# Optimization experiments

Measured on AMD Instinct MI355X. Metric: run time of the kernel, lower is better.

Reference implementation:

```python
import jax, jax.numpy as jnp
import numpy as np

H, DK, DV, SEG, D = 16, 64, 64, 512, 1024


def setup_inputs() -> dict:
    key = jax.random.key(0)
    ks = jax.random.split(key, 6)
    B, T = 2, 8192
    x = jax.random.normal(ks[0], (B, T, D), jnp.float32)
    Wq = jax.random.normal(ks[1], (H * DK, D), jnp.float32) * 0.02
    Wk = jax.random.normal(ks[2], (H * DK, D), jnp.float32) * 0.02
    Wv = jax.random.normal(ks[3], (H * DV, D), jnp.float32) * 0.02
    Wout = jax.random.normal(ks[4], (D, H * DV), jnp.float32) * 0.02
    betas = jax.random.normal(ks[5], (1, H, 1, DV), jnp.float32)
    return {"x": x, "Wq": Wq, "Wk": Wk, "Wv": Wv, "Wout": Wout, "betas": betas}


def reference(x, Wq, Wk, Wv, Wout, betas):
    B, T, _ = x.shape
    n_seg = T // SEG
    # Projections for the whole sequence, then PyTorch-style .view head split:
    # per segment, (B, SEG, H*dk).view(B, H, SEG, dk) is a raw row-major reshape.
    q = (x @ Wq.T).reshape(B, n_seg, H, SEG, DK)
    k = (x @ Wk.T).reshape(B, n_seg, H, SEG, DK)
    v = (x @ Wv.T).reshape(B, n_seg, H, SEG, DV)
    qs = jnp.moveaxis(q, 1, 0)  # (n_seg, B, H, SEG, DK)
    ks_ = jnp.moveaxis(k, 1, 0)
    vs = jnp.moveaxis(v, 1, 0)

    gate = jax.nn.sigmoid(betas)                 # (1, H, 1, DV)
    scale = 1.0 / jnp.sqrt(jnp.float32(DK))

    mem0 = jnp.zeros((B, H, DK, DV), x.dtype)
    # z broadcasts from (B,H,DV,1) to (B,H,DV,DK) on first update; start dense.
    z0 = jnp.zeros((B, H, DV, DK), x.dtype)

    def step(carry, seg):
        mem, z = carry
        q, k, v = seg
        sq = jax.nn.elu(q) + 1.0                 # (B,H,S,DK)
        sk = jax.nn.elu(k) + 1.0
        z = z + sk.sum(axis=-2, keepdims=True)   # (B,H,DV,DK) via broadcast
        scores = jnp.einsum('bhsd,bhtd->bhst', q, k) * scale
        att_dot = jnp.einsum('bhst,bhtv->bhsv', jax.nn.softmax(scores, axis=-1), v)
        att_mem = jnp.einsum('bhsd,bhdv->bhsv', sq, mem) / jnp.einsum('bhsd,bhdv->bhsv', sq, z)
        mem = mem + jnp.einsum('bhsd,bhsv->bhdv', sk, v)  # linear update (after att_mem)
        att = gate * att_mem + (1.0 - gate) * att_dot     # (B,H,S,DV)
        # PyTorch .view(B, SEG, H*DV) on (B,H,S,DV): raw reshape, no transpose.
        y = att.reshape(B, SEG, H * DV) @ Wout.T          # (B,SEG,D)
        return (mem, z), y

    (_, _), ys = jax.lax.scan(step, (mem0, z0), (qs, ks_, vs))
    out = jnp.moveaxis(ys, 0, 1).reshape(B, T, D)
    return out
```

## Files before the change

### kernel.cpp

```cpp
#include <hip/hip_runtime.h>


#define H_ 16
#define SEG_ 512
#define NSEG_ 16
#define B_ 2
#define T_ 8192
#define D_ 1024
#define BT_ 16384

#define NPROJ ((size_t)BT_ * D_)
#define NW ((size_t)D_ * D_)

__device__ unsigned short g_qb[NPROJ], g_kb[NPROJ], g_vb[NPROJ];
__device__ unsigned short g_xh[NPROJ];
__device__ unsigned short g_wqkv[3 * NW];
__device__ unsigned short g_ath[NPROJ], g_atl[NPROJ];
__device__ unsigned short g_woh[NW], g_wol[NW];
__device__ unsigned short g_vt[(size_t)512 * 64 * 512];
__device__ float g_M[(size_t)512 * 4096];
__device__ float g_z[(size_t)512 * 64];

typedef __attribute__((ext_vector_type(8))) short short8;
typedef __attribute__((ext_vector_type(8))) unsigned short ushort8;
typedef __attribute__((ext_vector_type(4))) float f32x4;

__device__ __forceinline__ float elu1(float x) {
    return x > 0.f ? x + 1.f : __expf(x);
}
__device__ __forceinline__ unsigned short f2bf(float x) {
    unsigned u = __float_as_uint(x);
    u += 0x7fffu + ((u >> 16) & 1u);
    return (unsigned short)(u >> 16);
}
__device__ __forceinline__ float bf2f(unsigned short h) {
    return __uint_as_float((unsigned)h << 16);
}
__device__ __forceinline__ void load_lds16(const unsigned short* g, unsigned short* l) {
    __builtin_amdgcn_global_load_lds(
        (const __attribute__((address_space(1))) unsigned int*)g,
        (__attribute__((address_space(3))) unsigned int*)l, 16, 0, 0);
}
__device__ __forceinline__ int sz8(int row, int blk) {
    return row * 64 + ((blk ^ (row & 7)) << 3);
}

__global__ __launch_bounds__(256) void prep_cast(
    const float* __restrict__ x, const float* __restrict__ Wq,
    const float* __restrict__ Wk, const float* __restrict__ Wv,
    const float* __restrict__ Wout,
    unsigned short* __restrict__ xh, unsigned short* __restrict__ wqkv,
    unsigned short* __restrict__ woh, unsigned short* __restrict__ wol)
{
    const int b = blockIdx.x;
    const int nXB = (int)(NPROJ / 1024);
    const int nWB = (int)(NW / 1024);
    if (b < nXB + 3 * nWB) {
        const float* in;
        unsigned short* out;
        int i;
        if (b < nXB) {
            in = x; out = xh; i = (b * 256 + threadIdx.x) * 4;
        } else {
            const int wsel = (b - nXB) / nWB;
            const int wb   = (b - nXB) % nWB;
            in  = wsel == 0 ? Wq : (wsel == 1 ? Wk : Wv);
            out = wqkv + (size_t)wsel * NW;
            i = (wb * 256 + threadIdx.x) * 4;
        }
        float4 v = *(const float4*)(in + i);
        ushort4 h;
        h.x = f2bf(v.x); h.y = f2bf(v.y); h.z = f2bf(v.z); h.w = f2bf(v.w);
        *(ushort4*)(out + i) = h;
    } else {
        const int wb = b - nXB - 3 * nWB;
        const int i = (wb * 256 + threadIdx.x) * 4;
        float4 v = *(const float4*)(Wout + i);
        ushort4 h, l;
        h.x = f2bf(v.x); l.x = f2bf(v.x - bf2f(h.x));
        h.y = f2bf(v.y); l.y = f2bf(v.y - bf2f(h.y));
        h.z = f2bf(v.z); l.z = f2bf(v.z - bf2f(h.z));
        h.w = f2bf(v.w); l.w = f2bf(v.w - bf2f(h.w));
        *(ushort4*)(woh + i) = h;
        *(ushort4*)(wol + i) = l;
    }
}


#define VMC(N) asm volatile("s_waitcnt vmcnt(" #N ")" ::: "memory")

#define STAGE_A(p, h, tt, u) \
    load_lds16(Aw + ((h) * 128 + (u) * 8) * 1024 + (tt) * 64, \
               &lds[(p) * 32768 + ((h) * 128 + w * 16 + (u) * 8) * 64])
#define STAGE_B(p, h, tt, u) \
    load_lds16(Bww + ((h) * 128 + (u) * 8) * 1024 + (tt) * 64, \
               &lds[(p) * 32768 + 16384 + ((h) * 128 + w * 16 + (u) * 8) * 64])
#define STAGE_AH(p, h, tt) do { STAGE_A(p, h, tt, 0); STAGE_A(p, h, tt, 1); } while (0)
#define STAGE_BH(p, h, tt) do { STAGE_B(p, h, tt, 0); STAGE_B(p, h, tt, 1); } while (0)

#define LDA(PBUF, MLO) do { \
    _Pragma("unroll") for (int m2 = 0; m2 < 4; ++m2) \
    _Pragma("unroll") for (int ks2 = 0; ks2 < 2; ++ks2) \
        a[m2][ks2] = *(const short8*)&lds[(PBUF) * 32768 + aoff[ks2] + ((MLO) + m2) * 1024]; \
} while (0)

#define LDB(PBUF) do { \
    _Pragma("unroll") for (int n2 = 0; n2 < 4; ++n2) \
    _Pragma("unroll") for (int ks2 = 0; ks2 < 2; ++ks2) \
        b[n2][ks2] = *(const short8*)&lds[(PBUF) * 32768 + boff[ks2] + n2 * 1024]; \
} while (0)

#define MFMA_QUAD(MLO, NLO) do { \
    _Pragma("unroll") for (int m2 = 0; m2 < 4; ++m2) \
    _Pragma("unroll") for (int n2 = 0; n2 < 2; ++n2) \
    _Pragma("unroll") for (int ks2 = 0; ks2 < 2; ++ks2) \
        acc[(MLO) + m2][(NLO) + n2] = __builtin_amdgcn_mfma_f32_16x16x32_bf16( \
            a[m2][ks2], b[(NLO) + n2][ks2], acc[(MLO) + m2][(NLO) + n2], 0, 0, 0); \
} while (0)

#define PH(MLO, NLO) do { \
    __builtin_amdgcn_s_barrier(); \
    asm volatile("s_waitcnt lgkmcnt(0)" ::: "memory"); \
    __builtin_amdgcn_sched_barrier(0); \
    __builtin_amdgcn_s_setprio(1); \
    MFMA_QUAD(MLO, NLO); \
    __builtin_amdgcn_s_setprio(0); \
    __builtin_amdgcn_sched_barrier(0); \
    __builtin_amdgcn_s_barrier(); \
} while (0)

__global__ __launch_bounds__(512, 2) void gemm_qkv8(
    const unsigned short* __restrict__ A, const unsigned short* __restrict__ Bw,
    unsigned short* __restrict__ Q, unsigned short* __restrict__ Kp,
    unsigned short* __restrict__ V)
{
    __shared__ unsigned short lds[65536];
    const int t = threadIdx.x, lane = t & 63, w = t >> 6;
    const int wave_m = w >> 2, wave_n = w & 3;

    const int bid = blockIdx.x;
    const int sb = (bid & 7) * 96 + (bid >> 3);
    const int mb = sb / 12, nb = sb % 12;
    const int m0 = mb * 256, n0 = nb * 256;

    const int lrow = lane >> 3;
    const int lcol = ((lane & 7) ^ lrow) * 8;
    const unsigned short* Aw  = A  + (size_t)(m0 + w * 16 + lrow) * 1024 + lcol;
    const unsigned short* Bww = Bw + (size_t)(n0 + w * 16 + lrow) * 1024 + lcol;

    const int fr = lane & 15, g4 = lane >> 4;
    int aoff[2], boff[2];
#pragma unroll
    for (int ks2 = 0; ks2 < 2; ++ks2) {
        aoff[ks2] = (wave_m * 128 + fr) * 64 + (((ks2 * 4 + g4) ^ (fr & 7)) * 8);
        boff[ks2] = 16384 + (wave_n * 64 + fr) * 64 + (((ks2 * 4 + g4) ^ (fr & 7)) * 8);
    }

    f32x4 acc[8][4];
#pragma unroll
    for (int i = 0; i < 8; ++i)
#pragma unroll
        for (int j = 0; j < 4; ++j) acc[i][j] = (f32x4)0.f;
    short8 a[4][2], b[4][2];

    STAGE_BH(0, 0, 0); STAGE_BH(0, 1, 0); STAGE_AH(0, 0, 0); STAGE_AH(0, 1, 0);
    STAGE_BH(1, 0, 1); STAGE_BH(1, 1, 1); STAGE_AH(1, 0, 1);
    VMC(6);
    __builtin_amdgcn_s_barrier();

#pragma unroll 1
    for (int it = 0; it < 7; ++it) {
        const int t1 = 2 * it + 1, t2 = 2 * it + 2, t3 = 2 * it + 3;
        LDB(0); LDA(0, 0);
        STAGE_AH(1, 1, t1);
        PH(0, 0);
        STAGE_BH(0, 0, t2);
        PH(0, 2);
        LDA(0, 4);
        STAGE_BH(0, 1, t2);
        PH(4, 0);
        STAGE_AH(0, 0, t2);
        VMC(6);
        PH(4, 2);
        LDB(1); LDA(1, 0);
        STAGE_AH(0, 1, t2);
        PH(0, 0);
        STAGE_BH(1, 0, t3);
        PH(0, 2);
        LDA(1, 4);
        STAGE_BH(1, 1, t3);
        PH(4, 0);
        STAGE_AH(1, 0, t3);
        VMC(6);
        PH(4, 2);
    }
    LDB(0); LDA(0, 0);
    STAGE_AH(1, 1, 15);
    PH(0, 0);
    PH(0, 2);
    LDA(0, 4);
    PH(4, 0);
    VMC(0);
    PH(4, 2);
    LDB(1); LDA(1, 0);
    PH(0, 0);
    PH(0, 2);
    LDA(1, 4);
    PH(4, 0);
    PH(4, 2);

    const int ccol = lane & 15, crow = (lane >> 4) * 4;
#pragma unroll
    for (int m = 0; m < 8; ++m)
#pragma unroll
        for (int n = 0; n < 4; ++n) {
            const int col = wave_n * 64 + n * 16 + ccol;
            const int cb = col >> 3, cl = col & 7;
#pragma unroll
            for (int r = 0; r < 4; ++r) {
                const int row = wave_m * 128 + m * 16 + crow + r;
                lds[row * 256 + ((cb ^ (row & 31)) << 3) + cl] = f2bf(acc[m][n][r]);
            }
        }
    __syncthreads();
    const int which = n0 >> 10, col0 = n0 & 1023;
    unsigned short* outp = which == 0 ? Q : (which == 1 ? Kp : V);
    const int orow = t >> 1, och = (t & 1) * 128;
    unsigned short* gp = outp + (size_t)(m0 + orow) * 1024 + col0 + och;
#pragma unroll
    for (int u = 0; u < 128; u += 8) {
        const int bo = (och + u) >> 3;
        *(ushort8*)(gp + u) = *(const ushort8*)&lds[orow * 256 + ((bo ^ (orow & 31)) << 3)];
    }
}


#define OSTG(p, arrp, aroff, tt, u) \
    load_lds16(arrp + (size_t)(u) * 16 * 1024 + (tt) * 32, \
               &lds[(p) * 32768 + (aroff) + (w * 32 + (u) * 16) * 32])
#define OUNIT(p, arrp, aroff, tt) do { OSTG(p, arrp, aroff, tt, 0); OSTG(p, arrp, aroff, tt, 1); } while (0)

#define OLDA(PBUF, MLO) do { \
    _Pragma("unroll") for (int m2 = 0; m2 < 4; ++m2) { \
        ah[m2] = *(const short8*)&lds[(PBUF) * 32768 +         ao + ((MLO) + m2) * 512]; \
        al[m2] = *(const short8*)&lds[(PBUF) * 32768 +  8192 + ao + ((MLO) + m2) * 512]; \
    } \
} while (0)

#define OLDB(PBUF) do { \
    _Pragma("unroll") for (int n2 = 0; n2 < 4; ++n2) { \
        bh[n2] = *(const short8*)&lds[(PBUF) * 32768 + 16384 + bo + n2 * 512]; \
        bl[n2] = *(const short8*)&lds[(PBUF) * 32768 + 24576 + bo + n2 * 512]; \
    } \
} while (0)

#define OQUAD(MLO, NLO) do { \
    _Pragma("unroll") for (int m2 = 0; m2 < 4; ++m2) \
    _Pragma("unroll") for (int n2 = 0; n2 < 2; ++n2) { \
        acc[(MLO) + m2][(NLO) + n2] = __builtin_amdgcn_mfma_f32_16x16x32_bf16( \
            ah[m2], bh[(NLO) + n2], acc[(MLO) + m2][(NLO) + n2], 0, 0, 0); \
        acc[(MLO) + m2][(NLO) + n2] = __builtin_amdgcn_mfma_f32_16x16x32_bf16( \
            al[m2], bh[(NLO) + n2], acc[(MLO) + m2][(NLO) + n2], 0, 0, 0); \
        acc[(MLO) + m2][(NLO) + n2] = __builtin_amdgcn_mfma_f32_16x16x32_bf16( \
            ah[m2], bl[(NLO) + n2], acc[(MLO) + m2][(NLO) + n2], 0, 0, 0); \
    } \
} while (0)

#define OPH(MLO, NLO) do { \
    __builtin_amdgcn_s_barrier(); \
    asm volatile("s_waitcnt lgkmcnt(0)" ::: "memory"); \
    __builtin_amdgcn_sched_barrier(0); \
    __builtin_amdgcn_s_setprio(1); \
    OQUAD(MLO, NLO); \
    __builtin_amdgcn_s_setprio(0); \
    __builtin_amdgcn_sched_barrier(0); \
    __builtin_amdgcn_s_barrier(); \
} while (0)

__global__ __launch_bounds__(512, 2) void gemm_bt8(
    const unsigned short* __restrict__ Ah, const unsigned short* __restrict__ Al,
    const unsigned short* __restrict__ Bh, const unsigned short* __restrict__ Bl,
    float* __restrict__ C)
{
    __shared__ unsigned short lds[65536];
    const int t = threadIdx.x, lane = t & 63, w = t >> 6;
    const int wave_m = w >> 2, wave_n = w & 3;

    const int bid = blockIdx.x;
    const int sb = (bid & 7) * 32 + (bid >> 3);
    const int m0 = (sb >> 2) * 256, n0 = (sb & 3) * 256;

    const int lrow = lane >> 2;
    const int lcol = ((lane & 3) ^ ((lane >> 3) & 3)) * 8;
    const unsigned short* Ahp = Ah + (size_t)(m0 + w * 32 + lrow) * 1024 + lcol;
    const unsigned short* Alp = Al + (size_t)(m0 + w * 32 + lrow) * 1024 + lcol;
    const unsigned short* Bhp = Bh + (size_t)(n0 + w * 32 + lrow) * 1024 + lcol;
    const unsigned short* Blp = Bl + (size_t)(n0 + w * 32 + lrow) * 1024 + lcol;

    const int fr = lane & 15, g4 = lane >> 4;
    const int xo = (g4 ^ ((fr >> 1) & 3)) * 8;
    const int ao = (wave_m * 128 + fr) * 32 + xo;
    const int bo = (wave_n * 64 + fr) * 32 + xo;

    f32x4 acc[8][4];
#pragma unroll
    for (int i = 0; i < 8; ++i)
#pragma unroll
        for (int j = 0; j < 4; ++j) acc[i][j] = (f32x4)0.f;
    short8 ah[4], al[4], bh[4], bl[4];

    OUNIT(0, Bhp, 16384, 0); OUNIT(0, Blp, 24576, 0); OUNIT(0, Ahp, 0, 0); OUNIT(0, Alp, 8192, 0);
    OUNIT(1, Bhp, 16384, 1); OUNIT(1, Blp, 24576, 1); OUNIT(1, Ahp, 0, 1);
    VMC(6);
    __builtin_amdgcn_s_barrier();

#pragma unroll 1
    for (int it = 0; it < 15; ++it) {
        const int t1 = 2 * it + 1, t2 = 2 * it + 2, t3 = 2 * it + 3;
        OLDB(0); OLDA(0, 0);
        OUNIT(1, Alp, 8192, t1);
        OPH(0, 0);
        OUNIT(0, Bhp, 16384, t2);
        OPH(0, 2);
        OLDA(0, 4);
        OUNIT(0, Blp, 24576, t2);
        OPH(4, 0);
        OUNIT(0, Ahp, 0, t2);
        VMC(6);
        OPH(4, 2);
        OLDB(1); OLDA(1, 0);
        OUNIT(0, Alp, 8192, t2);
        OPH(0, 0);
        OUNIT(1, Bhp, 16384, t3);
        OPH(0, 2);
        OLDA(1, 4);
        OUNIT(1, Blp, 24576, t3);
        OPH(4, 0);
        OUNIT(1, Ahp, 0, t3);
        VMC(6);
        OPH(4, 2);
    }
    OLDB(0); OLDA(0, 0);
    OUNIT(1, Alp, 8192, 31);
    OPH(0, 0);
    OPH(0, 2);
    OLDA(0, 4);
    OPH(4, 0);
    VMC(0);
    OPH(4, 2);
    OLDB(1); OLDA(1, 0);
    OPH(0, 0);
    OPH(0, 2);
    OLDA(1, 4);
    OPH(4, 0);
    OPH(4, 2);

    const int ccol = lane & 15, crow = (lane >> 4) * 4;
#pragma unroll
    for (int m = 0; m < 8; ++m)
#pragma unroll
        for (int n = 0; n < 4; ++n) {
            float* cp = C + (size_t)(m0 + wave_m * 128 + m * 16 + crow) * 1024
                          + (n0 + wave_n * 64 + n * 16 + ccol);
#pragma unroll
            for (int r = 0; r < 4; ++r) cp[(size_t)r * 1024] = acc[m][n][r];
        }
}

__global__ __launch_bounds__(256) void seg_stats(
    const unsigned short* __restrict__ kproj, const unsigned short* __restrict__ vproj,
    float* __restrict__ Mseg, float* __restrict__ zsum,
    unsigned short* __restrict__ vtg)
{
    __shared__ float ks[64][68];
    __shared__ float vs[64][68];
    const int idx = blockIdx.x;
    const int seg = idx & 15;
    const int bh  = idx >> 4;
    const int h   = bh & 15;
    const int b   = bh >> 4;
    const size_t base = ((size_t)b * T_ + (size_t)seg * SEG_ + (size_t)h * 32) * D_;
    const unsigned short* kt = kproj + base;
    const unsigned short* vt = vproj + base;
    const int t  = threadIdx.x;
    const int d0 = (t >> 4) * 4;
    const int v0 = (t & 15) * 4;
    const int lr = t >> 2;
    const int lc = (t & 3) * 16;
    float acc[4][4];
#pragma unroll
    for (int i = 0; i < 4; ++i)
#pragma unroll
        for (int j = 0; j < 4; ++j) acc[i][j] = 0.f;
    float zacc = 0.f;

    for (int c0 = 0; c0 < SEG_; c0 += 64) {
        __syncthreads();
        {
            const unsigned short* kp = kt + (size_t)(c0 + lr) * 64 + lc;
            const unsigned short* vp = vt + (size_t)(c0 + lr) * 64 + lc;
            ushort8 k0 = *(const ushort8*)kp,       k1 = *(const ushort8*)(kp + 8);
            ushort8 v0v = *(const ushort8*)vp,      v1 = *(const ushort8*)(vp + 8);
#pragma unroll
            for (int e = 0; e < 8; ++e) {
                ks[lr][lc + e]     = elu1(bf2f(k0[e]));
                ks[lr][lc + 8 + e] = elu1(bf2f(k1[e]));
                vs[lr][lc + e]     = bf2f(v0v[e]);
                vs[lr][lc + 8 + e] = bf2f(v1[e]);
            }
        }
        __syncthreads();
#pragma unroll 8
        for (int i = 0; i < 64; ++i) {
            float a0 = ks[i][d0 + 0], a1 = ks[i][d0 + 1];
            float a2 = ks[i][d0 + 2], a3 = ks[i][d0 + 3];
            float b0 = vs[i][v0 + 0], b1 = vs[i][v0 + 1];
            float b2 = vs[i][v0 + 2], b3 = vs[i][v0 + 3];
            acc[0][0] += a0 * b0; acc[0][1] += a0 * b1; acc[0][2] += a0 * b2; acc[0][3] += a0 * b3;
            acc[1][0] += a1 * b0; acc[1][1] += a1 * b1; acc[1][2] += a1 * b2; acc[1][3] += a1 * b3;
            acc[2][0] += a2 * b0; acc[2][1] += a2 * b1; acc[2][2] += a2 * b2; acc[2][3] += a2 * b3;
            acc[3][0] += a3 * b0; acc[3][1] += a3 * b1; acc[3][2] += a3 * b2; acc[3][3] += a3 * b3;
        }
        if (t < 64) {
#pragma unroll 8
            for (int i = 0; i < 64; ++i) zacc += ks[i][t];
        }
        {
            ushort8 w0, w1;
#pragma unroll
            for (int i = 0; i < 8; ++i) w0[i] = f2bf(vs[lc + i][lr]);
#pragma unroll
            for (int i = 0; i < 8; ++i) w1[i] = f2bf(vs[lc + 8 + i][lr]);
            unsigned short* vo = vtg + ((size_t)idx * 64 + lr) * 512 + c0 + lc;
            *(ushort8*)vo       = w0;
            *(ushort8*)(vo + 8) = w1;
        }
    }
    float* Mout = Mseg + (size_t)idx * 4096;
#pragma unroll
    for (int i = 0; i < 4; ++i)
        *(float4*)(Mout + (size_t)(d0 + i) * 64 + v0) =
            make_float4(acc[i][0], acc[i][1], acc[i][2], acc[i][3]);
    if (t < 64) zsum[(size_t)idx * 64 + t] = zacc;
}

__global__ __launch_bounds__(256) void prefix_scan(
    float* __restrict__ M, float* __restrict__ z)
{
    const int blk = blockIdx.x;
    const int bh  = blk >> 2, sl = blk & 3;
    const int t   = threadIdx.x;
    const size_t off = (size_t)bh * NSEG_ * 4096 + (size_t)sl * 1024 + (size_t)t * 4;
    float4 run = make_float4(0.f, 0.f, 0.f, 0.f);
    float runz = 0.f;
    for (int seg = 0; seg < NSEG_; ++seg) {
        const size_t o = off + (size_t)seg * 4096;
        float4 m = *(const float4*)(M + o);
        *(float4*)(M + o) = run;
        run.x += m.x; run.y += m.y; run.z += m.z; run.w += m.w;
        if (sl == 0 && t < 64) {
            const size_t oz = ((size_t)bh * NSEG_ + seg) * 64 + t;
            runz += z[oz];
            z[oz] = runz;
        }
    }
}

__global__ __launch_bounds__(256) void attn_mfma(
    const unsigned short* __restrict__ qproj, const unsigned short* __restrict__ kproj,
    const unsigned short* __restrict__ vtg, const float* __restrict__ memb,
    const float* __restrict__ Zaf, const float* __restrict__ betas,
    unsigned short* __restrict__ ath, unsigned short* __restrict__ atl)
{
    __shared__ unsigned short sm_k[64 * 64];
    __shared__ unsigned short sm_v[64 * 64];
    __shared__ unsigned short sm_p[64 * 64];
    __shared__ float Zsh[64], gsh[64];

    const int idx  = blockIdx.x;
    const int qc   = (idx >> 3) & 7;
    const int rest = (idx >> 6) * 8 + (idx & 7);
    const int bh   = rest >> 4;
    const int seg  = rest & 15;
    const int h    = bh & 15;
    const int b    = bh >> 4;
    const size_t base = ((size_t)b * T_ + (size_t)seg * SEG_ + (size_t)h * 32) * D_;

    const int t    = threadIdx.x;
    const int lane = t & 63;
    const int w    = t >> 6;
    const int c16  = lane & 15;
    const int g4   = lane >> 4;
    const int lr   = t >> 2;
    const int lc   = (t & 3) * 16;

    const unsigned short* qt = qproj + base + (size_t)qc * 4096;
    const unsigned short* kt = kproj + base;
    const unsigned short* vt = vtg + (size_t)rest * (64 * 512);
    const float* mb = memb + (size_t)rest * 4096;

    if (t < 64) {
        Zsh[t] = Zaf[(size_t)rest * 64 + t];
        gsh[t] = 1.f / (1.f + __expf(-betas[h * 64 + t]));
    }

    short8 qh[2], sqh[2];
    float rowsum = 0.f;
#pragma unroll
    for (int ks = 0; ks < 2; ++ks) {
        const unsigned short* qp = qt + (size_t)(w * 16 + c16) * 64 + g4 * 8 + ks * 32;
        ushort8 qv = *(const ushort8*)qp;
        short8 qf, sf;
#pragma unroll
        for (int j = 0; j < 8; ++j) {
            float e = elu1(bf2f(qv[j]));
            rowsum += e;
            qf[j] = (short)qv[j];
            sf[j] = (short)f2bf(e);
        }
        qh[ks] = qf; sqh[ks] = sf;
    }
    rowsum += __shfl_xor(rowsum, 16);
    rowsum += __shfl_xor(rowsum, 32);

    {
        const float* mp = mb + (size_t)lr * 64 + lc;
#pragma unroll
        for (int u = 0; u < 4; ++u) {
            float4 m4 = *(const float4*)(mp + u * 4);
            sm_p[sz8(lc + u * 4 + 0, lr >> 3) + (lr & 7)] = f2bf(m4.x);
            sm_p[sz8(lc + u * 4 + 1, lr >> 3) + (lr & 7)] = f2bf(m4.y);
            sm_p[sz8(lc + u * 4 + 2, lr >> 3) + (lr & 7)] = f2bf(m4.z);
            sm_p[sz8(lc + u * 4 + 3, lr >> 3) + (lr & 7)] = f2bf(m4.w);
        }
    }
    __syncthreads();

    f32x4 numf[4];
#pragma unroll
    for (int nf = 0; nf < 4; ++nf) numf[nf] = (f32x4)0.f;
#pragma unroll
    for (int ks = 0; ks < 2; ++ks)
#pragma unroll
        for (int nf = 0; nf < 4; ++nf) {
            short8 bm = *(const short8*)&sm_p[sz8(nf * 16 + c16, g4 + ks * 4)];
            numf[nf] = __builtin_amdgcn_mfma_f32_16x16x32_bf16(sqh[ks], bm, numf[nf], 0, 0, 0);
        }

    short8 bones;
#pragma unroll
    for (int j = 0; j < 8; ++j) bones[j] = (short)0x3F80;

    f32x4 o[4];
#pragma unroll
    for (int nf = 0; nf < 4; ++nf) o[nf] = (f32x4)0.f;
    float mrow[4] = {-1e30f, -1e30f, -1e30f, -1e30f};
    float lrow[4] = {0.f, 0.f, 0.f, 0.f};

    for (int kb = 0; kb < 8; ++kb) {
        __syncthreads();
        {
            const unsigned short* kp = kt + (size_t)(kb * 64 + lr) * 64 + lc;
            *(ushort8*)&sm_k[sz8(lr, lc >> 3)]       = *(const ushort8*)kp;
            *(ushort8*)&sm_k[sz8(lr, (lc >> 3) + 1)] = *(const ushort8*)(kp + 8);
            const unsigned short* vp = vt + (size_t)lr * 512 + kb * 64 + lc;
            *(ushort8*)&sm_v[sz8(lr, lc >> 3)]       = *(const ushort8*)vp;
            *(ushort8*)&sm_v[sz8(lr, (lc >> 3) + 1)] = *(const ushort8*)(vp + 8);
        }
        __syncthreads();

        f32x4 s[4];
#pragma unroll
        for (int nf = 0; nf < 4; ++nf) s[nf] = (f32x4)0.f;
#pragma unroll
        for (int ks = 0; ks < 2; ++ks)
#pragma unroll
            for (int nf = 0; nf < 4; ++nf) {
                short8 bk = *(const short8*)&sm_k[sz8(nf * 16 + c16, g4 + ks * 4)];
                s[nf] = __builtin_amdgcn_mfma_f32_16x16x32_bf16(qh[ks], bk, s[nf], 0, 0, 0);
            }
#pragma unroll
        for (int nf = 0; nf < 4; ++nf) s[nf] *= 0.125f;

        float pmax[4];
#pragma unroll
        for (int r = 0; r < 4; ++r)
            pmax[r] = fmaxf(fmaxf(s[0][r], s[1][r]), fmaxf(s[2][r], s[3][r]));
        const bool ok = pmax[0] <= mrow[0] + 8.f && pmax[1] <= mrow[1] + 8.f &&
                        pmax[2] <= mrow[2] + 8.f && pmax[3] <= mrow[3] + 8.f;
        if (!__all(ok)) {
#pragma unroll
            for (int r = 0; r < 4; ++r) {
                float mx = pmax[r];
                mx = fmaxf(mx, __shfl_xor(mx, 1));
                mx = fmaxf(mx, __shfl_xor(mx, 2));
                mx = fmaxf(mx, __shfl_xor(mx, 4));
                mx = fmaxf(mx, __shfl_xor(mx, 8));
                const float mnew = fmaxf(mrow[r], mx);
                const float corr = __expf(mrow[r] - mnew);
                mrow[r] = mnew;
                lrow[r] *= corr;
#pragma unroll
                for (int nf = 0; nf < 4; ++nf) o[nf][r] *= corr;
            }
        }
#pragma unroll
        for (int nf = 0; nf < 4; ++nf)
#pragma unroll
            for (int r = 0; r < 4; ++r) {
                s[nf][r] = __expf(s[nf][r] - mrow[r]);
                sm_p[sz8(w * 16 + g4 * 4 + r, nf * 2 + (c16 >> 3)) + (c16 & 7)] =
                    f2bf(s[nf][r]);
            }

        f32x4 psum = (f32x4)0.f;
#pragma unroll
        for (int ks = 0; ks < 2; ++ks) {
            short8 pa = *(const short8*)&sm_p[sz8(w * 16 + c16, g4 + ks * 4)];
            psum = __builtin_amdgcn_mfma_f32_16x16x32_bf16(pa, bones, psum, 0, 0, 0);
#pragma unroll
            for (int nf = 0; nf < 4; ++nf) {
                short8 bv = *(const short8*)&sm_v[sz8(nf * 16 + c16, g4 + ks * 4)];
                o[nf] = __builtin_amdgcn_mfma_f32_16x16x32_bf16(pa, bv, o[nf], 0, 0, 0);
            }
        }
#pragma unroll
        for (int r = 0; r < 4; ++r) lrow[r] += psum[r];
    }

    __syncthreads();

    float rs[4], invl[4];
#pragma unroll
    for (int r = 0; r < 4; ++r) {
        rs[r]   = __shfl(rowsum, (g4 << 2) + r);
        invl[r] = 1.f / lrow[r];
    }
#pragma unroll
    for (int nf = 0; nf < 4; ++nf) {
        const int col = nf * 16 + c16;
        const float Zc = Zsh[col], gc = gsh[col];
        const float izc = 1.f / Zc;
#pragma unroll
        for (int r = 0; r < 4; ++r) {
            const float adot = o[nf][r] * invl[r];
            const float amem = numf[nf][r] * izc / rs[r];
            const float res  = gc * amem + (1.f - gc) * adot;
            const unsigned short hv = f2bf(res);
            const unsigned short lv = f2bf(res - bf2f(hv));
            const int row = w * 16 + g4 * 4 + r;
            const int so  = sz8(row, nf * 2 + (c16 >> 3)) + (c16 & 7);
            sm_k[so] = hv;
            sm_v[so] = lv;
        }
    }
    __syncthreads();
    {
        const size_t ob = base + (size_t)(qc * 64 + lr) * 64 + lc;
        *(ushort8*)(ath + ob)     = *(const ushort8*)&sm_k[sz8(lr, lc >> 3)];
        *(ushort8*)(ath + ob + 8) = *(const ushort8*)&sm_k[sz8(lr, (lc >> 3) + 1)];
        *(ushort8*)(atl + ob)     = *(const ushort8*)&sm_v[sz8(lr, lc >> 3)];
        *(ushort8*)(atl + ob + 8) = *(const ushort8*)&sm_v[sz8(lr, (lc >> 3) + 1)];
    }
}

extern "C" void kernel_launch(void* const* d_in, const int* in_sizes, int n_in,
                              void* d_out, int out_size, void* d_ws, size_t ws_size,
                              hipStream_t stream) {
    const float* x     = (const float*)d_in[0];
    const float* Wq    = (const float*)d_in[1];
    const float* Wk    = (const float*)d_in[2];
    const float* Wv    = (const float*)d_in[3];
    const float* Wout  = (const float*)d_in[4];
    const float* betas = (const float*)d_in[5];
    float* out = (float*)d_out;
    (void)d_ws; (void)ws_size;

    float *M, *z;
    unsigned short *qb, *kb, *vb, *xh, *wqkv, *vt, *ath, *atl, *woh, *wol;
    hipGetSymbolAddress((void**)&qb,   HIP_SYMBOL(g_qb));
    hipGetSymbolAddress((void**)&kb,   HIP_SYMBOL(g_kb));
    hipGetSymbolAddress((void**)&vb,   HIP_SYMBOL(g_vb));
    hipGetSymbolAddress((void**)&xh,   HIP_SYMBOL(g_xh));
    hipGetSymbolAddress((void**)&wqkv, HIP_SYMBOL(g_wqkv));
    hipGetSymbolAddress((void**)&vt,   HIP_SYMBOL(g_vt));
    hipGetSymbolAddress((void**)&ath,  HIP_SYMBOL(g_ath));
    hipGetSymbolAddress((void**)&atl,  HIP_SYMBOL(g_atl));
    hipGetSymbolAddress((void**)&woh,  HIP_SYMBOL(g_woh));
    hipGetSymbolAddress((void**)&wol,  HIP_SYMBOL(g_wol));
    hipGetSymbolAddress((void**)&M,    HIP_SYMBOL(g_M));
    hipGetSymbolAddress((void**)&z,    HIP_SYMBOL(g_z));

    const int nXB = (int)(NPROJ / 1024), nWB = (int)(NW / 1024);
    prep_cast<<<nXB + 4 * nWB, 256, 0, stream>>>(x, Wq, Wk, Wv, Wout,
                                                 xh, wqkv, woh, wol);

    gemm_qkv8<<<dim3(768), 512, 0, stream>>>(xh, wqkv, qb, kb, vb);
    seg_stats<<<B_ * H_ * NSEG_, 256, 0, stream>>>(kb, vb, M, z, vt);
    prefix_scan<<<B_ * H_ * 4, 256, 0, stream>>>(M, z);
    attn_mfma<<<B_ * H_ * NSEG_ * 8, 256, 0, stream>>>(qb, kb, vt, M, z, betas, ath, atl);
    gemm_bt8<<<dim3(256), 512, 0, stream>>>(ath, atl, woh, wol, out);
}
```

Measured before the change: 502.4 us.

## Compute segment K^T V statistics with bf16 MFMA using hi/lo split

The seg_stats kernel now computes the per-segment K^T V outer-product sum and the key column sums with bf16 MFMA instructions instead of scalar FP32 FMAs out of shared memory. elu(k)+1 is split into high and low bf16 parts to keep near-FP32 accuracy, the column sum is done as an MFMA against a vector of ones, and V is staged transposed in a swizzled bf16 layout that is reused for the V-transpose write. This cuts scalar ALU work and shared-memory traffic in a small kernel, at the cost of extra MFMAs for the lo term and a slight accuracy change.

Result: faster. 485.8 us (-3.3%).

```diff
diff --git a/kernel.cpp b/kernel.cpp
--- a/kernel.cpp
+++ b/kernel.cpp
@@ -372,8 +372,9 @@
     float* __restrict__ Mseg, float* __restrict__ zsum,
     unsigned short* __restrict__ vtg)
 {
-    __shared__ float ks[64][68];
-    __shared__ float vs[64][68];
+    __shared__ unsigned short sm_kh[64 * 64];
+    __shared__ unsigned short sm_kl[64 * 64];
+    __shared__ unsigned short sm_vt[64 * 64];
     const int idx = blockIdx.x;
     const int seg = idx & 15;
     const int bh  = idx >> 4;
@@ -382,66 +383,75 @@
     const size_t base = ((size_t)b * T_ + (size_t)seg * SEG_ + (size_t)h * 32) * D_;
     const unsigned short* kt = kproj + base;
     const unsigned short* vt = vproj + base;
-    const int t  = threadIdx.x;
-    const int d0 = (t >> 4) * 4;
-    const int v0 = (t & 15) * 4;
-    const int lr = t >> 2;
-    const int lc = (t & 3) * 16;
-    float acc[4][4];
-#pragma unroll
-    for (int i = 0; i < 4; ++i)
-#pragma unroll
-        for (int j = 0; j < 4; ++j) acc[i][j] = 0.f;
-    float zacc = 0.f;
+    const int t    = threadIdx.x;
+    const int lane = t & 63;
+    const int w    = t >> 6;
+    const int c16  = lane & 15;
+    const int g4   = lane >> 4;
+    const int lr   = t >> 2;
+    const int lc   = (t & 3) * 16;
+
+    short8 bones;
+#pragma unroll
+    for (int j = 0; j < 8; ++j) bones[j] = (short)0x3F80;
+
+    f32x4 acc[4];
+#pragma unroll
+    for (int nt = 0; nt < 4; ++nt) acc[nt] = (f32x4)0.f;
+    f32x4 zacc = (f32x4)0.f;
 
     for (int c0 = 0; c0 < SEG_; c0 += 64) {
         __syncthreads();
         {
-            const unsigned short* kp = kt + (size_t)(c0 + lr) * 64 + lc;
-            const unsigned short* vp = vt + (size_t)(c0 + lr) * 64 + lc;
-            ushort8 k0 = *(const ushort8*)kp,       k1 = *(const ushort8*)(kp + 8);
-            ushort8 v0v = *(const ushort8*)vp,      v1 = *(const ushort8*)(vp + 8);
+            const int row = c0 + lane;
+            const unsigned short* kp = kt + (size_t)row * 64 + w * 16;
+            const unsigned short* vp = vt + (size_t)row * 64 + w * 16;
+            ushort8 k0 = *(const ushort8*)kp, k1 = *(const ushort8*)(kp + 8);
+            ushort8 v0 = *(const ushort8*)vp, v1 = *(const ushort8*)(vp + 8);
+            const int tb = lane >> 3, tl = lane & 7;
 #pragma unroll
             for (int e = 0; e < 8; ++e) {
-                ks[lr][lc + e]     = elu1(bf2f(k0[e]));
-                ks[lr][lc + 8 + e] = elu1(bf2f(k1[e]));
-                vs[lr][lc + e]     = bf2f(v0v[e]);
-                vs[lr][lc + 8 + e] = bf2f(v1[e]);
+                const float f0 = elu1(bf2f(k0[e]));
+                const unsigned short h0 = f2bf(f0), l0 = f2bf(f0 - bf2f(h0));
+                const float f1 = elu1(bf2f(k1[e]));
+                const unsigned short h1 = f2bf(f1), l1 = f2bf(f1 - bf2f(h1));
+                const int a0 = sz8(w * 16 + e,     tb) + tl;
+                const int a1 = sz8(w * 16 + 8 + e, tb) + tl;
+                sm_kh[a0] = h0; sm_kl[a0] = l0; sm_vt[a0] = v0[e];
+                sm_kh[a1] = h1; sm_kl[a1] = l1; sm_vt[a1] = v1[e];
             }
         }
         __syncthreads();
-#pragma unroll 8
-        for (int i = 0; i < 64; ++i) {
-            float a0 = ks[i][d0 + 0], a1 = ks[i][d0 + 1];
-            float a2 = ks[i][d0 + 2], a3 = ks[i][d0 + 3];
-            float b0 = vs[i][v0 + 0], b1 = vs[i][v0 + 1];
-            float b2 = vs[i][v0 + 2], b3 = vs[i][v0 + 3];
-            acc[0][0] += a0 * b0; acc[0][1] += a0 * b1; acc[0][2] += a0 * b2; acc[0][3] += a0 * b3;
-            acc[1][0] += a1 * b0; acc[1][1] += a1 * b1; acc[1][2] += a1 * b2; acc[1][3] += a1 * b3;
-            acc[2][0] += a2 * b0; acc[2][1] += a2 * b1; acc[2][2] += a2 * b2; acc[2][3] += a2 * b3;
-            acc[3][0] += a3 * b0; acc[3][1] += a3 * b1; acc[3][2] += a3 * b2; acc[3][3] += a3 * b3;
-        }
-        if (t < 64) {
-#pragma unroll 8
-            for (int i = 0; i < 64; ++i) zacc += ks[i][t];
+#pragma unroll
+        for (int ks = 0; ks < 2; ++ks) {
+            const short8 ahh = *(const short8*)&sm_kh[sz8(w * 16 + c16, ks * 4 + g4)];
+            const short8 alo = *(const short8*)&sm_kl[sz8(w * 16 + c16, ks * 4 + g4)];
+            zacc = __builtin_amdgcn_mfma_f32_16x16x32_bf16(ahh, bones, zacc, 0, 0, 0);
+            zacc = __builtin_amdgcn_mfma_f32_16x16x32_bf16(alo, bones, zacc, 0, 0, 0);
+#pragma unroll
+            for (int nt = 0; nt < 4; ++nt) {
+                const short8 bv = *(const short8*)&sm_vt[sz8(nt * 16 + c16, ks * 4 + g4)];
+                acc[nt] = __builtin_amdgcn_mfma_f32_16x16x32_bf16(ahh, bv, acc[nt], 0, 0, 0);
+                acc[nt] = __builtin_amdgcn_mfma_f32_16x16x32_bf16(alo, bv, acc[nt], 0, 0, 0);
+            }
         }
         {
-            ushort8 w0, w1;
-#pragma unroll
-            for (int i = 0; i < 8; ++i) w0[i] = f2bf(vs[lc + i][lr]);
-#pragma unroll
-            for (int i = 0; i < 8; ++i) w1[i] = f2bf(vs[lc + 8 + i][lr]);
             unsigned short* vo = vtg + ((size_t)idx * 64 + lr) * 512 + c0 + lc;
-            *(ushort8*)vo       = w0;
-            *(ushort8*)(vo + 8) = w1;
+            *(ushort8*)vo       = *(const ushort8*)&sm_vt[sz8(lr, lc >> 3)];
+            *(ushort8*)(vo + 8) = *(const ushort8*)&sm_vt[sz8(lr, (lc >> 3) + 1)];
         }
     }
     float* Mout = Mseg + (size_t)idx * 4096;
 #pragma unroll
-    for (int i = 0; i < 4; ++i)
-        *(float4*)(Mout + (size_t)(d0 + i) * 64 + v0) =
-            make_float4(acc[i][0], acc[i][1], acc[i][2], acc[i][3]);
-    if (t < 64) zsum[(size_t)idx * 64 + t] = zacc;
+    for (int nt = 0; nt < 4; ++nt)
+#pragma unroll
+        for (int r = 0; r < 4; ++r)
+            Mout[(size_t)(w * 16 + g4 * 4 + r) * 64 + nt * 16 + c16] = acc[nt][r];
+    if (c16 == 0) {
+#pragma unroll
+        for (int r = 0; r < 4; ++r)
+            zsum[(size_t)idx * 64 + w * 16 + g4 * 4 + r] = zacc[r];
+    }
 }
 
 __global__ __launch_bounds__(256) void prefix_scan(
```
